# Kernel optimization log

Hardware: AMD Instinct MI355X
Metric: run time of the kernel (lower is better)

Reference implementation:

```python
import jax, jax.numpy as jnp
import numpy as np

N_NODES = 200000
D = 256
HID = 512
OUT = 2
NUM_GRAPHS = 512


def setup_inputs() -> dict:
    key = jax.random.key(0)
    ks = jax.random.split(key, 8)
    x = jax.random.normal(ks[0], (N_NODES, D), dtype=jnp.float32)
    batch = jnp.sort(jax.random.randint(ks[1], (N_NODES,), 0, NUM_GRAPHS, dtype=jnp.int32))
    # MLP params (Linear stores weight as [out, in] in torch; we use [in, out])
    W1 = jax.random.normal(ks[2], (D, HID), dtype=jnp.float32) / np.sqrt(D)
    b1 = jnp.zeros((HID,), dtype=jnp.float32)
    W2 = jax.random.normal(ks[3], (HID, HID), dtype=jnp.float32) / np.sqrt(HID)
    b2 = jnp.zeros((HID,), dtype=jnp.float32)
    W3 = jax.random.normal(ks[4], (HID, OUT), dtype=jnp.float32) / np.sqrt(HID)
    b3 = jnp.zeros((OUT,), dtype=jnp.float32)
    return {"final_node_embeddings": x, "batch_vector": batch,
            "W1": W1, "b1": b1, "W2": W2, "b2": b2, "W3": W3, "b3": b3}


def reference(final_node_embeddings, batch_vector, W1, b1, W2, b2, W3, b3):
    x = final_node_embeddings
    # segment max pooling over graphs; empty graphs -> zeros (matches original)
    seg = jax.ops.segment_max(x, batch_vector, num_segments=NUM_GRAPHS)  # [G, D]
    counts = jax.ops.segment_sum(jnp.ones((x.shape[0],), dtype=x.dtype),
                                 batch_vector, num_segments=NUM_GRAPHS)  # [G]
    g = jnp.where(counts[:, None] > 0, seg, jnp.zeros((), dtype=x.dtype))
    # readout MLP (dropout inactive at inference)
    h = jax.nn.relu(g @ W1 + b1)
    h = jax.nn.relu(h @ W2 + b2)
    return h @ W3 + b3
```

## Files before the change

kernel.cpp:

```cpp
#include <hip/hip_runtime.h>
#include <float.h>

#define N_NODES 200000
#define D 256
#define HID 512
#define OUTD 2
#define NG 512

__global__ void k_bounds(const int* __restrict__ batch, int* __restrict__ row_start, int n) {
    int i = blockIdx.x * blockDim.x + threadIdx.x;
    if (i >= n) return;
    int b  = batch[i];
    int bp = (i == 0) ? -1 : batch[i - 1];
    for (int g = bp + 1; g <= b; ++g) row_start[g] = i;
    if (i == n - 1) {
        for (int g = b + 1; g <= NG; ++g) row_start[g] = n;
    }
}

__global__ __launch_bounds__(256) void k_pool(const float* __restrict__ x,
                                              const int* __restrict__ row_start,
                                              float* __restrict__ gp) {
    const int g    = blockIdx.x;
    const int lane = threadIdx.x & 63;
    const int wave = threadIdx.x >> 6;
    const int r0 = row_start[g];
    const int r1 = row_start[g + 1];

    float4 m = make_float4(-FLT_MAX, -FLT_MAX, -FLT_MAX, -FLT_MAX);
    const float* xc = x + (size_t)lane * 4;

    int r = r0 + wave;
    for (; r + 12 < r1; r += 16) {
        float4 v0 = *reinterpret_cast<const float4*>(xc + (size_t)r * D);
        float4 v1 = *reinterpret_cast<const float4*>(xc + (size_t)(r + 4) * D);
        float4 v2 = *reinterpret_cast<const float4*>(xc + (size_t)(r + 8) * D);
        float4 v3 = *reinterpret_cast<const float4*>(xc + (size_t)(r + 12) * D);
        m.x = fmaxf(m.x, fmaxf(fmaxf(v0.x, v1.x), fmaxf(v2.x, v3.x)));
        m.y = fmaxf(m.y, fmaxf(fmaxf(v0.y, v1.y), fmaxf(v2.y, v3.y)));
        m.z = fmaxf(m.z, fmaxf(fmaxf(v0.z, v1.z), fmaxf(v2.z, v3.z)));
        m.w = fmaxf(m.w, fmaxf(fmaxf(v0.w, v1.w), fmaxf(v2.w, v3.w)));
    }
    for (; r < r1; r += 4) {
        float4 v = *reinterpret_cast<const float4*>(xc + (size_t)r * D);
        m.x = fmaxf(m.x, v.x); m.y = fmaxf(m.y, v.y);
        m.z = fmaxf(m.z, v.z); m.w = fmaxf(m.w, v.w);
    }

    __shared__ float4 lds[4][64];
    lds[wave][lane] = m;
    __syncthreads();
    if (wave == 0) {
        float4 a = lds[0][lane], b = lds[1][lane], c = lds[2][lane], d = lds[3][lane];
        float4 o;
        o.x = fmaxf(fmaxf(a.x, b.x), fmaxf(c.x, d.x));
        o.y = fmaxf(fmaxf(a.y, b.y), fmaxf(c.y, d.y));
        o.z = fmaxf(fmaxf(a.z, b.z), fmaxf(c.z, d.z));
        o.w = fmaxf(fmaxf(a.w, b.w), fmaxf(c.w, d.w));
        if (r1 == r0) o = make_float4(0.f, 0.f, 0.f, 0.f);
        *reinterpret_cast<float4*>(gp + (size_t)g * D + lane * 4) = o;
    }
}

template <int K, bool RELU>
__global__ __launch_bounds__(256) void k_gemm(const float* __restrict__ A,
                                              const float* __restrict__ B,
                                              const float* __restrict__ bias,
                                              float* __restrict__ C, int N) {
    __shared__ float As[32][33];
    __shared__ float Bs[32][33];
    const int t  = threadIdx.x;
    const int bm = blockIdx.y * 32;
    const int bn = blockIdx.x * 32;
    const int lr = t >> 3;
    const int lc = (t & 7) << 2;
    const int tx = t & 15;
    const int ty = t >> 4;
    float acc00 = 0.f, acc01 = 0.f, acc10 = 0.f, acc11 = 0.f;

    for (int k0 = 0; k0 < K; k0 += 32) {
        float4 av = *reinterpret_cast<const float4*>(A + (size_t)(bm + lr) * K + k0 + lc);
        float4 bv = *reinterpret_cast<const float4*>(B + (size_t)(k0 + lr) * N + bn + lc);
        __syncthreads();
        As[lr][lc] = av.x; As[lr][lc + 1] = av.y; As[lr][lc + 2] = av.z; As[lr][lc + 3] = av.w;
        Bs[lr][lc] = bv.x; Bs[lr][lc + 1] = bv.y; Bs[lr][lc + 2] = bv.z; Bs[lr][lc + 3] = bv.w;
        __syncthreads();
#pragma unroll
        for (int kk = 0; kk < 32; ++kk) {
            float a0 = As[ty * 2][kk], a1 = As[ty * 2 + 1][kk];
            float b0 = Bs[kk][tx * 2], b1 = Bs[kk][tx * 2 + 1];
            acc00 += a0 * b0; acc01 += a0 * b1;
            acc10 += a1 * b0; acc11 += a1 * b1;
        }
    }

    const int r = bm + ty * 2, c = bn + tx * 2;
    float bc0 = bias[c], bc1 = bias[c + 1];
    float v00 = acc00 + bc0, v01 = acc01 + bc1;
    float v10 = acc10 + bc0, v11 = acc11 + bc1;
    if (RELU) {
        v00 = fmaxf(v00, 0.f); v01 = fmaxf(v01, 0.f);
        v10 = fmaxf(v10, 0.f); v11 = fmaxf(v11, 0.f);
    }
    C[(size_t)r * N + c]           = v00;
    C[(size_t)r * N + c + 1]       = v01;
    C[(size_t)(r + 1) * N + c]     = v10;
    C[(size_t)(r + 1) * N + c + 1] = v11;
}

__global__ __launch_bounds__(256) void k_fc3(const float* __restrict__ h,
                                             const float* __restrict__ W,
                                             const float* __restrict__ b,
                                             float* __restrict__ out) {
    const int wave = threadIdx.x >> 6;
    const int lane = threadIdx.x & 63;
    const int e = blockIdx.x * 4 + wave;
    const int row = e >> 1, col = e & 1;
    float s = 0.f;
#pragma unroll
    for (int k = lane; k < HID; k += 64)
        s += h[(size_t)row * HID + k] * W[(size_t)k * OUTD + col];
#pragma unroll
    for (int off = 32; off; off >>= 1) s += __shfl_xor(s, off);
    if (lane == 0) out[e] = s + b[col];
}

extern "C" void kernel_launch(void* const* d_in, const int* in_sizes, int n_in,
                              void* d_out, int out_size, void* d_ws, size_t ws_size,
                              hipStream_t stream) {
    const float* x     = (const float*)d_in[0];
    const int*   batch = (const int*)d_in[1];
    const float* W1    = (const float*)d_in[2];
    const float* b1    = (const float*)d_in[3];
    const float* W2    = (const float*)d_in[4];
    const float* b2    = (const float*)d_in[5];
    const float* W3    = (const float*)d_in[6];
    const float* b3    = (const float*)d_in[7];
    float* out = (float*)d_out;

    char* ws = (char*)d_ws;
    int*   row_start = (int*)ws;
    float* gp = (float*)(ws + 4096);
    float* h1 = (float*)(ws + 4096 + 512 * 1024);
    float* h2 = (float*)(ws + 4096 + 512 * 1024 + 1024 * 1024);

    k_bounds<<<(N_NODES + 255) / 256, 256, 0, stream>>>(batch, row_start, N_NODES);
    k_pool<<<NG, 256, 0, stream>>>(x, row_start, gp);
    k_gemm<D,   true ><<<dim3(HID / 32, NG / 32), 256, 0, stream>>>(gp, W1, b1, h1, HID);
    k_gemm<HID, true ><<<dim3(HID / 32, NG / 32), 256, 0, stream>>>(h1, W2, b2, h2, HID);
    k_fc3<<<NG * OUTD / 4, 256, 0, stream>>>(h2, W3, b3, out);
}
```

Measured before the change: 67.70 us.

## Fuse segment bounds search into pool kernel and use 4x4 register-tiled GEMM

Drops the separate k_bounds launch. Each pool block now finds its own segment start and end with a wave-wide 64-ary lower-bound search over the sorted batch vector. The GEMM kernels switch from 256 threads computing 2x2 outputs to 64 threads computing 4x4 outputs each, with a transposed A tile and float4 LDS reads and stores. This removes one launch plus a full pass over the batch array and raises arithmetic per LDS access. In exchange, each GEMM block has fewer threads, which lowers latency hiding, and every pool block repeats a small search.

Measured after the change: 75.55 us. +11.6%, slower.

```diff
diff --git a/kernel.cpp b/kernel.cpp
--- a/kernel.cpp
+++ b/kernel.cpp
@@ -7,25 +7,38 @@
 #define OUTD 2
 #define NG 512
 
-__global__ void k_bounds(const int* __restrict__ batch, int* __restrict__ row_start, int n) {
-    int i = blockIdx.x * blockDim.x + threadIdx.x;
-    if (i >= n) return;
-    int b  = batch[i];
-    int bp = (i == 0) ? -1 : batch[i - 1];
-    for (int g = bp + 1; g <= b; ++g) row_start[g] = i;
-    if (i == n - 1) {
-        for (int g = b + 1; g <= NG; ++g) row_start[g] = n;
+__device__ __forceinline__ int lower_bound_64ary(const int* __restrict__ a, int n,
+                                                 int v, int lane) {
+    int lo = -1, hi = n;
+    while (hi - lo > 1) {
+        int len = hi - lo;
+        int off = 1 + (int)(((long long)lane * (len - 1)) >> 6);
+        int p = lo + off;
+        bool lt = a[p] < v;
+        unsigned long long m = __ballot(lt);
+        int cnt = __popcll(m);
+        int nlo = (cnt == 0) ? lo : lo + 1 + (int)(((long long)(cnt - 1) * (len - 1)) >> 6);
+        int nhi = (cnt == 64) ? hi : lo + 1 + (int)(((long long)cnt * (len - 1)) >> 6);
+        lo = nlo; hi = nhi;
     }
+    return hi;
 }
 
 __global__ __launch_bounds__(256) void k_pool(const float* __restrict__ x,
-                                              const int* __restrict__ row_start,
+                                              const int* __restrict__ batch,
                                               float* __restrict__ gp) {
     const int g    = blockIdx.x;
     const int lane = threadIdx.x & 63;
     const int wave = threadIdx.x >> 6;
-    const int r0 = row_start[g];
-    const int r1 = row_start[g + 1];
+
+    __shared__ int sb[2];
+    if (wave < 2) {
+        int r = lower_bound_64ary(batch, N_NODES, g + wave, lane);
+        if (lane == 0) sb[wave] = r;
+    }
+    __syncthreads();
+    const int r0 = sb[0];
+    const int r1 = sb[1];
 
     float4 m = make_float4(-FLT_MAX, -FLT_MAX, -FLT_MAX, -FLT_MAX);
     const float* xc = x + (size_t)lane * 4;
@@ -63,49 +76,68 @@
 }
 
 template <int K, bool RELU>
-__global__ __launch_bounds__(256) void k_gemm(const float* __restrict__ A,
-                                              const float* __restrict__ B,
-                                              const float* __restrict__ bias,
-                                              float* __restrict__ C, int N) {
-    __shared__ float As[32][33];
-    __shared__ float Bs[32][33];
+__global__ __launch_bounds__(64) void k_gemm(const float* __restrict__ A,
+                                             const float* __restrict__ B,
+                                             const float* __restrict__ bias,
+                                             float* __restrict__ C, int N) {
+    __shared__ float AsT[32][36];
+    __shared__ float Bs[32][36];
     const int t  = threadIdx.x;
     const int bm = blockIdx.y * 32;
     const int bn = blockIdx.x * 32;
-    const int lr = t >> 3;
-    const int lc = (t & 7) << 2;
-    const int tx = t & 15;
-    const int ty = t >> 4;
-    float acc00 = 0.f, acc01 = 0.f, acc10 = 0.f, acc11 = 0.f;
+    const int r  = t >> 1;
+    const int h  = t & 1;
+    const int ty = t >> 3;
+    const int tx = t & 7;
+
+    float acc[4][4] = {};
 
     for (int k0 = 0; k0 < K; k0 += 32) {
-        float4 av = *reinterpret_cast<const float4*>(A + (size_t)(bm + lr) * K + k0 + lc);
-        float4 bv = *reinterpret_cast<const float4*>(B + (size_t)(k0 + lr) * N + bn + lc);
+        float4 a4[4], b4[4];
+#pragma unroll
+        for (int j = 0; j < 4; ++j) {
+            a4[j] = *reinterpret_cast<const float4*>(A + (size_t)(bm + r) * K + k0 + h * 16 + j * 4);
+            b4[j] = *reinterpret_cast<const float4*>(B + (size_t)(k0 + r) * N + bn + h * 16 + j * 4);
+        }
         __syncthreads();
-        As[lr][lc] = av.x; As[lr][lc + 1] = av.y; As[lr][lc + 2] = av.z; As[lr][lc + 3] = av.w;
-        Bs[lr][lc] = bv.x; Bs[lr][lc + 1] = bv.y; Bs[lr][lc + 2] = bv.z; Bs[lr][lc + 3] = bv.w;
+#pragma unroll
+        for (int j = 0; j < 4; ++j) {
+            AsT[h * 16 + j * 4 + 0][r] = a4[j].x;
+            AsT[h * 16 + j * 4 + 1][r] = a4[j].y;
+            AsT[h * 16 + j * 4 + 2][r] = a4[j].z;
+            AsT[h * 16 + j * 4 + 3][r] = a4[j].w;
+            *reinterpret_cast<float4*>(&Bs[r][h * 16 + j * 4]) = b4[j];
+        }
         __syncthreads();
 #pragma unroll
         for (int kk = 0; kk < 32; ++kk) {
-            float a0 = As[ty * 2][kk], a1 = As[ty * 2 + 1][kk];
-            float b0 = Bs[kk][tx * 2], b1 = Bs[kk][tx * 2 + 1];
-            acc00 += a0 * b0; acc01 += a0 * b1;
-            acc10 += a1 * b0; acc11 += a1 * b1;
+            float4 a = *reinterpret_cast<const float4*>(&AsT[kk][ty * 4]);
+            float4 b = *reinterpret_cast<const float4*>(&Bs[kk][tx * 4]);
+            const float av[4] = {a.x, a.y, a.z, a.w};
+            const float bv[4] = {b.x, b.y, b.z, b.w};
+#pragma unroll
+            for (int i = 0; i < 4; ++i)
+#pragma unroll
+                for (int j = 0; j < 4; ++j)
+                    acc[i][j] += av[i] * bv[j];
         }
     }
 
-    const int r = bm + ty * 2, c = bn + tx * 2;
-    float bc0 = bias[c], bc1 = bias[c + 1];
-    float v00 = acc00 + bc0, v01 = acc01 + bc1;
-    float v10 = acc10 + bc0, v11 = acc11 + bc1;
-    if (RELU) {
-        v00 = fmaxf(v00, 0.f); v01 = fmaxf(v01, 0.f);
-        v10 = fmaxf(v10, 0.f); v11 = fmaxf(v11, 0.f);
+    float4 bb = *reinterpret_cast<const float4*>(bias + bn + tx * 4);
+    const float bvv[4] = {bb.x, bb.y, bb.z, bb.w};
+#pragma unroll
+    for (int i = 0; i < 4; ++i) {
+        float4 v;
+        v.x = acc[i][0] + bvv[0];
+        v.y = acc[i][1] + bvv[1];
+        v.z = acc[i][2] + bvv[2];
+        v.w = acc[i][3] + bvv[3];
+        if (RELU) {
+            v.x = fmaxf(v.x, 0.f); v.y = fmaxf(v.y, 0.f);
+            v.z = fmaxf(v.z, 0.f); v.w = fmaxf(v.w, 0.f);
+        }
+        *reinterpret_cast<float4*>(C + (size_t)(bm + ty * 4 + i) * N + bn + tx * 4) = v;
     }
-    C[(size_t)r * N + c]           = v00;
-    C[(size_t)r * N + c + 1]       = v01;
-    C[(size_t)(r + 1) * N + c]     = v10;
-    C[(size_t)(r + 1) * N + c + 1] = v11;
 }
 
 __global__ __launch_bounds__(256) void k_fc3(const float* __restrict__ h,
@@ -139,14 +171,12 @@
     float* out = (float*)d_out;
 
     char* ws = (char*)d_ws;
-    int*   row_start = (int*)ws;
-    float* gp = (float*)(ws + 4096);
-    float* h1 = (float*)(ws + 4096 + 512 * 1024);
-    float* h2 = (float*)(ws + 4096 + 512 * 1024 + 1024 * 1024);
+    float* gp = (float*)ws;
+    float* h1 = (float*)(ws + 512 * 1024);
+    float* h2 = (float*)(ws + 512 * 1024 + 1024 * 1024);
 
-    k_bounds<<<(N_NODES + 255) / 256, 256, 0, stream>>>(batch, row_start, N_NODES);
-    k_pool<<<NG, 256, 0, stream>>>(x, row_start, gp);
-    k_gemm<D,   true ><<<dim3(HID / 32, NG / 32), 256, 0, stream>>>(gp, W1, b1, h1, HID);
-    k_gemm<HID, true ><<<dim3(HID / 32, NG / 32), 256, 0, stream>>>(h1, W2, b2, h2, HID);
+    k_pool<<<NG, 256, 0, stream>>>(x, batch, gp);
+    k_gemm<D,   true ><<<dim3(HID / 32, NG / 32), 64, 0, stream>>>(gp, W1, b1, h1, HID);
+    k_gemm<HID, true ><<<dim3(HID / 32, NG / 32), 64, 0, stream>>>(h1, W2, b2, h2, HID);
     k_fc3<<<NG * OUTD / 4, 256, 0, stream>>>(h2, W3, b3, out);
 }
```

## Fuse segment-max pooling and full readout MLP into one per-graph-pair kernel

Applied to the files above, without the earlier changes.

Replaces the separate pooling, two tiled GEMM and final-projection kernels with one kernel in which each block pools two graphs into LDS and then runs all three MLP layers on them. Intermediate activations stay in shared memory, which removes global round-trips for the pooled rows and hidden layers and cuts three kernel launches. The pooling loop is also unrolled deeper, to eight loads in flight per wave. In exchange, every block re-reads all of W1 and W2 from cache, and only 256 blocks stream x, which may lower memory-level parallelism during the bandwidth-bound pooling phase.

New measurement: 66.84 us. About the same (-1.3%).

```diff
diff --git a/kernel.cpp b/kernel.cpp
--- a/kernel.cpp
+++ b/kernel.cpp
@@ -18,111 +18,138 @@
     }
 }
 
-__global__ __launch_bounds__(256) void k_pool(const float* __restrict__ x,
-                                              const int* __restrict__ row_start,
-                                              float* __restrict__ gp) {
-    const int g    = blockIdx.x;
-    const int lane = threadIdx.x & 63;
-    const int wave = threadIdx.x >> 6;
-    const int r0 = row_start[g];
-    const int r1 = row_start[g + 1];
-
-    float4 m = make_float4(-FLT_MAX, -FLT_MAX, -FLT_MAX, -FLT_MAX);
-    const float* xc = x + (size_t)lane * 4;
-
-    int r = r0 + wave;
-    for (; r + 12 < r1; r += 16) {
-        float4 v0 = *reinterpret_cast<const float4*>(xc + (size_t)r * D);
-        float4 v1 = *reinterpret_cast<const float4*>(xc + (size_t)(r + 4) * D);
-        float4 v2 = *reinterpret_cast<const float4*>(xc + (size_t)(r + 8) * D);
-        float4 v3 = *reinterpret_cast<const float4*>(xc + (size_t)(r + 12) * D);
-        m.x = fmaxf(m.x, fmaxf(fmaxf(v0.x, v1.x), fmaxf(v2.x, v3.x)));
-        m.y = fmaxf(m.y, fmaxf(fmaxf(v0.y, v1.y), fmaxf(v2.y, v3.y)));
-        m.z = fmaxf(m.z, fmaxf(fmaxf(v0.z, v1.z), fmaxf(v2.z, v3.z)));
-        m.w = fmaxf(m.w, fmaxf(fmaxf(v0.w, v1.w), fmaxf(v2.w, v3.w)));
-    }
-    for (; r < r1; r += 4) {
-        float4 v = *reinterpret_cast<const float4*>(xc + (size_t)r * D);
-        m.x = fmaxf(m.x, v.x); m.y = fmaxf(m.y, v.y);
-        m.z = fmaxf(m.z, v.z); m.w = fmaxf(m.w, v.w);
-    }
-
-    __shared__ float4 lds[4][64];
-    lds[wave][lane] = m;
-    __syncthreads();
-    if (wave == 0) {
-        float4 a = lds[0][lane], b = lds[1][lane], c = lds[2][lane], d = lds[3][lane];
-        float4 o;
-        o.x = fmaxf(fmaxf(a.x, b.x), fmaxf(c.x, d.x));
-        o.y = fmaxf(fmaxf(a.y, b.y), fmaxf(c.y, d.y));
-        o.z = fmaxf(fmaxf(a.z, b.z), fmaxf(c.z, d.z));
-        o.w = fmaxf(fmaxf(a.w, b.w), fmaxf(c.w, d.w));
-        if (r1 == r0) o = make_float4(0.f, 0.f, 0.f, 0.f);
-        *reinterpret_cast<float4*>(gp + (size_t)g * D + lane * 4) = o;
-    }
+__device__ __forceinline__ float4 fmax4(float4 a, float4 b) {
+    return make_float4(fmaxf(a.x, b.x), fmaxf(a.y, b.y), fmaxf(a.z, b.z), fmaxf(a.w, b.w));
 }
 
-template <int K, bool RELU>
-__global__ __launch_bounds__(256) void k_gemm(const float* __restrict__ A,
-                                              const float* __restrict__ B,
-                                              const float* __restrict__ bias,
-                                              float* __restrict__ C, int N) {
-    __shared__ float As[32][33];
-    __shared__ float Bs[32][33];
-    const int t  = threadIdx.x;
-    const int bm = blockIdx.y * 32;
-    const int bn = blockIdx.x * 32;
-    const int lr = t >> 3;
-    const int lc = (t & 7) << 2;
-    const int tx = t & 15;
-    const int ty = t >> 4;
-    float acc00 = 0.f, acc01 = 0.f, acc10 = 0.f, acc11 = 0.f;
+__global__ __launch_bounds__(256) void k_main(const float* __restrict__ x,
+                                              const int* __restrict__ rs,
+                                              const float* __restrict__ W1,
+                                              const float* __restrict__ b1,
+                                              const float* __restrict__ W2,
+                                              const float* __restrict__ b2,
+                                              const float* __restrict__ W3,
+                                              const float* __restrict__ b3,
+                                              float* __restrict__ out) {
+    const int t    = threadIdx.x;
+    const int lane = t & 63;
+    const int wave = t >> 6;
+    const int g0   = blockIdx.x * 2;
 
-    for (int k0 = 0; k0 < K; k0 += 32) {
-        float4 av = *reinterpret_cast<const float4*>(A + (size_t)(bm + lr) * K + k0 + lc);
-        float4 bv = *reinterpret_cast<const float4*>(B + (size_t)(k0 + lr) * N + bn + lc);
+    __shared__ float g_row[2][D];
+    __shared__ float h1s[2][HID];
+    __shared__ float h2s[2][HID];
+    __shared__ float4 red[4][64];
+    __shared__ float fin[4][4];
+
+    const float* xc = x + (size_t)lane * 4;
+#pragma unroll
+    for (int gi = 0; gi < 2; ++gi) {
+        const int r0 = rs[g0 + gi];
+        const int r1 = rs[g0 + gi + 1];
+        float4 m = make_float4(-FLT_MAX, -FLT_MAX, -FLT_MAX, -FLT_MAX);
+        int r = r0 + wave;
+        for (; r + 28 < r1; r += 32) {
+            float4 v0 = *reinterpret_cast<const float4*>(xc + (size_t)(r)      * D);
+            float4 v1 = *reinterpret_cast<const float4*>(xc + (size_t)(r + 4)  * D);
+            float4 v2 = *reinterpret_cast<const float4*>(xc + (size_t)(r + 8)  * D);
+            float4 v3 = *reinterpret_cast<const float4*>(xc + (size_t)(r + 12) * D);
+            float4 v4 = *reinterpret_cast<const float4*>(xc + (size_t)(r + 16) * D);
+            float4 v5 = *reinterpret_cast<const float4*>(xc + (size_t)(r + 20) * D);
+            float4 v6 = *reinterpret_cast<const float4*>(xc + (size_t)(r + 24) * D);
+            float4 v7 = *reinterpret_cast<const float4*>(xc + (size_t)(r + 28) * D);
+            m = fmax4(m, fmax4(fmax4(fmax4(v0, v1), fmax4(v2, v3)),
+                               fmax4(fmax4(v4, v5), fmax4(v6, v7))));
+        }
+        for (; r < r1; r += 4) {
+            float4 v = *reinterpret_cast<const float4*>(xc + (size_t)r * D);
+            m = fmax4(m, v);
+        }
         __syncthreads();
-        As[lr][lc] = av.x; As[lr][lc + 1] = av.y; As[lr][lc + 2] = av.z; As[lr][lc + 3] = av.w;
-        Bs[lr][lc] = bv.x; Bs[lr][lc + 1] = bv.y; Bs[lr][lc + 2] = bv.z; Bs[lr][lc + 3] = bv.w;
+        red[wave][lane] = m;
         __syncthreads();
-#pragma unroll
-        for (int kk = 0; kk < 32; ++kk) {
-            float a0 = As[ty * 2][kk], a1 = As[ty * 2 + 1][kk];
-            float b0 = Bs[kk][tx * 2], b1 = Bs[kk][tx * 2 + 1];
-            acc00 += a0 * b0; acc01 += a0 * b1;
-            acc10 += a1 * b0; acc11 += a1 * b1;
+        if (wave == 0) {
+            float4 o = fmax4(fmax4(red[0][lane], red[1][lane]),
+                             fmax4(red[2][lane], red[3][lane]));
+            if (r1 == r0) o = make_float4(0.f, 0.f, 0.f, 0.f);
+            *reinterpret_cast<float4*>(&g_row[gi][lane * 4]) = o;
         }
     }
+    __syncthreads();
 
-    const int r = bm + ty * 2, c = bn + tx * 2;
-    float bc0 = bias[c], bc1 = bias[c + 1];
-    float v00 = acc00 + bc0, v01 = acc01 + bc1;
-    float v10 = acc10 + bc0, v11 = acc11 + bc1;
-    if (RELU) {
-        v00 = fmaxf(v00, 0.f); v01 = fmaxf(v01, 0.f);
-        v10 = fmaxf(v10, 0.f); v11 = fmaxf(v11, 0.f);
+    {
+        float a00 = 0.f, a01 = 0.f, a10 = 0.f, a11 = 0.f;
+        const float* w = W1 + 2 * t;
+#pragma unroll 8
+        for (int k = 0; k < D; k += 4) {
+            float4 ga = *reinterpret_cast<const float4*>(&g_row[0][k]);
+            float4 gb = *reinterpret_cast<const float4*>(&g_row[1][k]);
+            float2 w0 = *reinterpret_cast<const float2*>(w + (size_t)(k)     * HID);
+            float2 w1 = *reinterpret_cast<const float2*>(w + (size_t)(k + 1) * HID);
+            float2 w2 = *reinterpret_cast<const float2*>(w + (size_t)(k + 2) * HID);
+            float2 w3 = *reinterpret_cast<const float2*>(w + (size_t)(k + 3) * HID);
+            a00 += ga.x * w0.x; a01 += ga.x * w0.y; a10 += gb.x * w0.x; a11 += gb.x * w0.y;
+            a00 += ga.y * w1.x; a01 += ga.y * w1.y; a10 += gb.y * w1.x; a11 += gb.y * w1.y;
+            a00 += ga.z * w2.x; a01 += ga.z * w2.y; a10 += gb.z * w2.x; a11 += gb.z * w2.y;
+            a00 += ga.w * w3.x; a01 += ga.w * w3.y; a10 += gb.w * w3.x; a11 += gb.w * w3.y;
+        }
+        float2 bb = *reinterpret_cast<const float2*>(b1 + 2 * t);
+        *reinterpret_cast<float2*>(&h1s[0][2 * t]) =
+            make_float2(fmaxf(a00 + bb.x, 0.f), fmaxf(a01 + bb.y, 0.f));
+        *reinterpret_cast<float2*>(&h1s[1][2 * t]) =
+            make_float2(fmaxf(a10 + bb.x, 0.f), fmaxf(a11 + bb.y, 0.f));
     }
-    C[(size_t)r * N + c]           = v00;
-    C[(size_t)r * N + c + 1]       = v01;
-    C[(size_t)(r + 1) * N + c]     = v10;
-    C[(size_t)(r + 1) * N + c + 1] = v11;
-}
+    __syncthreads();
 
-__global__ __launch_bounds__(256) void k_fc3(const float* __restrict__ h,
-                                             const float* __restrict__ W,
-                                             const float* __restrict__ b,
-                                             float* __restrict__ out) {
-    const int wave = threadIdx.x >> 6;
-    const int lane = threadIdx.x & 63;
-    const int e = blockIdx.x * 4 + wave;
-    const int row = e >> 1, col = e & 1;
-    float s = 0.f;
+    {
+        float a00 = 0.f, a01 = 0.f, a10 = 0.f, a11 = 0.f;
+        const float* w = W2 + 2 * t;
+#pragma unroll 8
+        for (int k = 0; k < HID; k += 4) {
+            float4 ga = *reinterpret_cast<const float4*>(&h1s[0][k]);
+            float4 gb = *reinterpret_cast<const float4*>(&h1s[1][k]);
+            float2 w0 = *reinterpret_cast<const float2*>(w + (size_t)(k)     * HID);
+            float2 w1 = *reinterpret_cast<const float2*>(w + (size_t)(k + 1) * HID);
+            float2 w2 = *reinterpret_cast<const float2*>(w + (size_t)(k + 2) * HID);
+            float2 w3 = *reinterpret_cast<const float2*>(w + (size_t)(k + 3) * HID);
+            a00 += ga.x * w0.x; a01 += ga.x * w0.y; a10 += gb.x * w0.x; a11 += gb.x * w0.y;
+            a00 += ga.y * w1.x; a01 += ga.y * w1.y; a10 += gb.y * w1.x; a11 += gb.y * w1.y;
+            a00 += ga.z * w2.x; a01 += ga.z * w2.y; a10 += gb.z * w2.x; a11 += gb.z * w2.y;
+            a00 += ga.w * w3.x; a01 += ga.w * w3.y; a10 += gb.w * w3.x; a11 += gb.w * w3.y;
+        }
+        float2 bb = *reinterpret_cast<const float2*>(b2 + 2 * t);
+        *reinterpret_cast<float2*>(&h2s[0][2 * t]) =
+            make_float2(fmaxf(a00 + bb.x, 0.f), fmaxf(a01 + bb.y, 0.f));
+        *reinterpret_cast<float2*>(&h2s[1][2 * t]) =
+            make_float2(fmaxf(a10 + bb.x, 0.f), fmaxf(a11 + bb.y, 0.f));
+    }
+    __syncthreads();
+
+    {
+        float4 w = *reinterpret_cast<const float4*>(W3 + 4 * t);
+        float2 ha = *reinterpret_cast<const float2*>(&h2s[0][2 * t]);
+        float2 hb = *reinterpret_cast<const float2*>(&h2s[1][2 * t]);
+        float p00 = ha.x * w.x + ha.y * w.z;
+        float p01 = ha.x * w.y + ha.y * w.w;
+        float p10 = hb.x * w.x + hb.y * w.z;
+        float p11 = hb.x * w.y + hb.y * w.w;
 #pragma unroll
-    for (int k = lane; k < HID; k += 64)
-        s += h[(size_t)row * HID + k] * W[(size_t)k * OUTD + col];
-#pragma unroll
-    for (int off = 32; off; off >>= 1) s += __shfl_xor(s, off);
-    if (lane == 0) out[e] = s + b[col];
+        for (int off = 32; off; off >>= 1) {
+            p00 += __shfl_xor(p00, off);
+            p01 += __shfl_xor(p01, off);
+            p10 += __shfl_xor(p10, off);
+            p11 += __shfl_xor(p11, off);
+        }
+        if (lane == 0) {
+            fin[wave][0] = p00; fin[wave][1] = p01;
+            fin[wave][2] = p10; fin[wave][3] = p11;
+        }
+        __syncthreads();
+        if (t < 4) {
+            float s = fin[0][t] + fin[1][t] + fin[2][t] + fin[3][t];
+            out[(size_t)(g0 + (t >> 1)) * OUTD + (t & 1)] = s + b3[t & 1];
+        }
+    }
 }
 
 extern "C" void kernel_launch(void* const* d_in, const int* in_sizes, int n_in,
@@ -138,15 +165,8 @@
     const float* b3    = (const float*)d_in[7];
     float* out = (float*)d_out;
 
-    char* ws = (char*)d_ws;
-    int*   row_start = (int*)ws;
-    float* gp = (float*)(ws + 4096);
-    float* h1 = (float*)(ws + 4096 + 512 * 1024);
-    float* h2 = (float*)(ws + 4096 + 512 * 1024 + 1024 * 1024);
+    int* row_start = (int*)d_ws;
 
     k_bounds<<<(N_NODES + 255) / 256, 256, 0, stream>>>(batch, row_start, N_NODES);
-    k_pool<<<NG, 256, 0, stream>>>(x, row_start, gp);
-    k_gemm<D,   true ><<<dim3(HID / 32, NG / 32), 256, 0, stream>>>(gp, W1, b1, h1, HID);
-    k_gemm<HID, true ><<<dim3(HID / 32, NG / 32), 256, 0, stream>>>(h1, W2, b2, h2, HID);
-    k_fc3<<<NG * OUTD / 4, 256, 0, stream>>>(h2, W3, b3, out);
+    k_main<<<NG / 2, 256, 0, stream>>>(x, row_start, W1, b1, W2, b2, W3, b3, out);
 }
```
